# Performance work log

Measured on AMD Instinct MI355X. Metric: run time of the kernel, lower is better.

The kernel has to match this reference:

```python
import jax, jax.numpy as jnp
import numpy as np

B, T, F, H, E, L = 8192, 32, 64, 128, 16, 8


def _lstm_layer(x, wih, whh, bih, bhh):
    # x: [B, T, in]; weights in torch layout: wih [4H, in], whh [4H, H]
    b, t, _ = x.shape
    h_dim = whh.shape[1]
    pre = jnp.einsum('bti,gi->btg', x, wih) + bih + bhh  # [B, T, 4H]
    pre_t = jnp.swapaxes(pre, 0, 1)  # [T, B, 4H]

    def step(carry, p):
        h, c = carry
        g = p + h @ whh.T
        i, f, gg, o = jnp.split(g, 4, axis=-1)  # torch gate order: i, f, g, o
        i = jax.nn.sigmoid(i)
        f = jax.nn.sigmoid(f)
        gg = jnp.tanh(gg)
        o = jax.nn.sigmoid(o)
        c = f * c + i * gg
        h = o * jnp.tanh(c)
        return (h, c), h

    init = (jnp.zeros((b, h_dim), x.dtype), jnp.zeros((b, h_dim), x.dtype))
    _, ys = jax.lax.scan(step, init, pre_t)
    return jnp.swapaxes(ys, 0, 1)  # [B, T, H]


def setup_inputs() -> dict:
    key = jax.random.key(0)
    ks = jax.random.split(key, 32)

    def w(k, shape, fan_in):
        return (jax.random.uniform(k, shape, jnp.float32, -1.0, 1.0) / np.sqrt(fan_in)).astype(jnp.float32)

    inp = {
        'x_feat': jax.random.normal(ks[0], (B, T, 8), jnp.float32),
        'access_type': jax.random.randint(ks[1], (B, T), 0, 16),
        # MemoryPatternEncoder
        'de_w1': w(ks[2], (32, 8), 8), 'de_b1': w(ks[3], (32,), 8),
        'de_w2': w(ks[4], (F, 32), 32), 'de_b2': w(ks[5], (F,), 32),
        'embed': jax.random.normal(ks[6], (E, 16), jnp.float32),
        'comb_w': w(ks[7], (F, F + 16), F + 16), 'comb_b': w(ks[8], (F,), F + 16),
        # 2-layer LSTM (torch param layout)
        'lstm0_wih': w(ks[9], (4 * H, F), H), 'lstm0_whh': w(ks[10], (4 * H, H), H),
        'lstm0_bih': w(ks[11], (4 * H,), H), 'lstm0_bhh': w(ks[12], (4 * H,), H),
        'lstm1_wih': w(ks[13], (4 * H, H), H), 'lstm1_whh': w(ks[14], (4 * H, H), H),
        'lstm1_bih': w(ks[15], (4 * H,), H), 'lstm1_bhh': w(ks[16], (4 * H,), H),
        # delta_predictor: H -> H -> L
        'dp_w1': w(ks[17], (H, H), H), 'dp_b1': w(ks[18], (H,), H),
        'dp_w2': w(ks[19], (L, H), H), 'dp_b2': w(ks[20], (L,), H),
        # confidence_predictor: H -> H//2 -> L, sigmoid
        'cp_w1': w(ks[21], (H // 2, H), H), 'cp_b1': w(ks[22], (H // 2,), H),
        'cp_w2': w(ks[23], (L, H // 2), H // 2), 'cp_b2': w(ks[24], (L,), H // 2),
        # pattern_classifier: H -> 32 -> 4, softmax
        'pc_w1': w(ks[25], (32, H), H), 'pc_b1': w(ks[26], (32,), H),
        'pc_w2': w(ks[27], (4, 32), 32), 'pc_b2': w(ks[28], (4,), 32),
    }
    return inp


def reference(x_feat, access_type, de_w1, de_b1, de_w2, de_b2, embed, comb_w, comb_b,
              lstm0_wih, lstm0_whh, lstm0_bih, lstm0_bhh,
              lstm1_wih, lstm1_whh, lstm1_bih, lstm1_bhh,
              dp_w1, dp_b1, dp_w2, dp_b2, cp_w1, cp_b1, cp_w2, cp_b2,
              pc_w1, pc_b1, pc_w2, pc_b2):
    # --- MemoryPatternEncoder (batched over B, T) ---
    delta_feat = jax.nn.relu(x_feat @ de_w1.T + de_b1) @ de_w2.T + de_b2  # [B,T,F]
    access_feat = embed[access_type]  # [B,T,16]
    feats = jnp.concatenate([delta_feat, access_feat], axis=-1) @ comb_w.T + comb_b  # [B,T,F]

    # --- 2-layer LSTM (dropout inactive: inference/no_grad path) ---
    y0 = _lstm_layer(feats, lstm0_wih, lstm0_whh, lstm0_bih, lstm0_bhh)
    y1 = _lstm_layer(y0, lstm1_wih, lstm1_whh, lstm1_bih, lstm1_bhh)
    h = y1[:, -1, :]  # final hidden [B,H]

    # --- heads ---
    deltas = (jax.nn.relu(h @ dp_w1.T + dp_b1) @ dp_w2.T + dp_b2) * 1000000.0  # [B,L]
    conf = jax.nn.sigmoid(jax.nn.relu(h @ cp_w1.T + cp_b1) @ cp_w2.T + cp_b2)  # [B,L]
    probs = jax.nn.softmax(jax.nn.relu(h @ pc_w1.T + pc_b1) @ pc_w2.T + pc_b2, axis=-1)  # [B,4]
    return jnp.concatenate([deltas, conf, probs], axis=-1)  # [B, 2L+4]
```

## Files before the change

### kernel.cpp

```cpp
#include <hip/hip_runtime.h>
#include <hip/hip_bf16.h>

typedef short s8v __attribute__((ext_vector_type(8)));
typedef float f4v __attribute__((ext_vector_type(4)));

#define DEV __device__ __forceinline__

DEV unsigned short f2b(float f) {
  unsigned u = __builtin_bit_cast(unsigned, f);
  u += 0x7FFFu + ((u >> 16) & 1u);
  return (unsigned short)(u >> 16);
}
DEV float b2f(unsigned short s) {
  unsigned u = ((unsigned)s) << 16;
  return __builtin_bit_cast(float, u);
}
DEV float sigf(float x) { return __builtin_amdgcn_rcpf(1.f + __expf(-x)); }
DEV float tanhf_(float x) { return 1.f - 2.f * __builtin_amdgcn_rcpf(__expf(2.f * x) + 1.f); }

#define O_WHH0  0u
#define O_WHH1  131072u
#define O_WIH0  262144u
#define O_WIH1  327680u
#define O_B0    458752u
#define O_B1    460800u
#define O_WA    462848u
#define O_EMB2  471040u
#define O_BC    475136u
#define O_W1F   475392u
#define O_DP2T  532736u
#define O_FEATS 4733696u
#define O_Y0    38288128u

#define P_WHH   0
#define P_H0    131072
#define P_H1    139264
#define P_TOT   147456
#define P_HMID  0
#define P_HW2   29696
#define P_HPC   36864

DEV int orig_col(int c) { return 128 * ((c >> 4) & 3) + 16 * (c >> 6) + (c & 15); }

__global__ void prep_kernel(
    const float* de_w1, const float* de_b1, const float* de_w2, const float* de_b2,
    const float* embed, const float* comb_w, const float* comb_b,
    const float* w0ih, const float* w0hh, const float* b0ih, const float* b0hh,
    const float* w1ih, const float* w1hh, const float* b1ih, const float* b1hh,
    const float* dp_w1, const float* dp_w2, const float* cp_w1, const float* cp_w2,
    const float* pc_w1, const float* pc_w2, char* ws)
{
  unsigned short* wih0p = (unsigned short*)(ws + O_WIH0);
  unsigned short* whh0p = (unsigned short*)(ws + O_WHH0);
  unsigned short* wih1p = (unsigned short*)(ws + O_WIH1);
  unsigned short* whh1p = (unsigned short*)(ws + O_WHH1);
  float* b0p = (float*)(ws + O_B0);
  float* b1p = (float*)(ws + O_B1);
  float* Wa  = (float*)(ws + O_WA);
  float* bc  = (float*)(ws + O_BC);
  float* em2 = (float*)(ws + O_EMB2);
  unsigned short* w1f = (unsigned short*)(ws + O_W1F);
  float* dp2t = (float*)(ws + O_DP2T);
  float* cp2t = dp2t + 1024;
  float* pc2t = dp2t + 1536;

  const int T0 = 32768, T1 = T0 + 65536, T2 = T1 + 65536, T3 = T2 + 65536,
            T4 = T3 + 512, T5 = T4 + 512, T6 = T5 + 2048, T7 = T6 + 64,
            T8 = T7 + 1024, T9 = T8 + 28672, T10 = T9 + 1024, T11 = T10 + 512,
            T12 = T11 + 128;

  for (int idx = blockIdx.x * 256 + threadIdx.x; idx < T12; idx += gridDim.x * 256) {
    if (idx < T3) {
      int u, Kin; const float* src; unsigned short* dst;
      if (idx < T0)      { u = idx;      Kin = 64;  src = w0ih; dst = wih0p; }
      else if (idx < T1) { u = idx - T0; Kin = 128; src = w0hh; dst = whh0p; }
      else if (idx < T2) { u = idx - T1; Kin = 128; src = w1ih; dst = wih1p; }
      else               { u = idx - T2; Kin = 128; src = w1hh; dst = whh1p; }
      int j = u & 7, l = (u >> 3) & 63, nt = (u >> 9) & 31, kt = u >> 14;
      int c = 16 * nt + (l & 15);
      int k = 32 * kt + 8 * (l >> 4) + j;
      dst[u] = f2b(src[orig_col(c) * Kin + k]);
    } else if (idx < T5) {
      int u = idx - T3;
      if (u < 512) b0p[u] = b0ih[orig_col(u)] + b0hh[orig_col(u)];
      else { int c = u - 512; b1p[c] = b1ih[orig_col(c)] + b1hh[orig_col(c)]; }
    } else if (idx < T6) {
      int u = idx - T5, f = u >> 5, kk = u & 31;
      float a = 0.f;
      for (int f2 = 0; f2 < 64; f2++) a += comb_w[f * 80 + f2] * de_w2[f2 * 32 + kk];
      Wa[u] = a;
    } else if (idx < T7) {
      int f = idx - T6;
      float a = comb_b[f];
      for (int f2 = 0; f2 < 64; f2++) a += comb_w[f * 80 + f2] * de_b2[f2];
      bc[f] = a;
    } else if (idx < T8) {
      int u = idx - T7, e = u >> 6, f = u & 63;
      float a = 0.f;
      for (int j = 0; j < 16; j++) a += embed[e * 16 + j] * comb_w[f * 80 + 64 + j];
      em2[u] = a;
    } else if (idx < T9) {
      int u = idx - T8;
      int j = u & 7, l = (u >> 3) & 63, kt = (u >> 9) & 3, nt = u >> 11;
      int c = 16 * nt + (l & 15);
      int k = 32 * kt + 8 * (l >> 4) + j;
      float v;
      if (c < 128)      v = dp_w1[c * 128 + k];
      else if (c < 192) v = cp_w1[(c - 128) * 128 + k];
      else              v = pc_w1[(c - 192) * 128 + k];
      w1f[u] = f2b(v);
    }
    else if (idx < T10)   { int u = idx - T9;  int k = u >> 3, o = u & 7; dp2t[u] = dp_w2[o * 128 + k]; }
    else if (idx < T11)   { int u = idx - T10; int k = u >> 3, o = u & 7; cp2t[u] = cp_w2[o * 64 + k]; }
    else                  { int u = idx - T11; int k = u >> 2, o = u & 3; pc2t[u] = pc_w2[o * 32 + k]; }
  }
}

__global__ __launch_bounds__(256) void frontend_kernel(
    const float* __restrict__ x_feat, const int* __restrict__ acc_t,
    const float* __restrict__ de_w1, const float* __restrict__ de_b1,
    const char* __restrict__ ws, unsigned short* __restrict__ feats)
{
  __shared__ float sW1[256], sB1[32], sWa[2048], sBc[64], sE2T[1024];
  const float* Wa  = (const float*)(ws + O_WA);
  const float* bc  = (const float*)(ws + O_BC);
  const float* em2 = (const float*)(ws + O_EMB2);
  int tid = threadIdx.x;
  sW1[tid] = de_w1[tid];
  if (tid < 32) sB1[tid] = de_b1[tid];
  for (int i = tid; i < 2048; i += 256) sWa[i] = Wa[i];
  if (tid < 64) sBc[tid] = bc[tid];
  for (int i = tid; i < 1024; i += 256) sE2T[i] = em2[(i & 15) * 64 + (i >> 4)];
  __syncthreads();

  int g = blockIdx.x * 256 + tid;
  f4v x0 = ((const f4v*)(x_feat + (size_t)g * 8))[0];
  f4v x1 = ((const f4v*)(x_feat + (size_t)g * 8))[1];
  float xs[8];
#pragma unroll
  for (int i = 0; i < 4; i++) { xs[i] = x0[i]; xs[4 + i] = x1[i]; }
  int at = acc_t[g];

  float r1[32];
#pragma unroll
  for (int kk = 0; kk < 32; kk++) {
    float a = sB1[kk];
#pragma unroll
    for (int i = 0; i < 8; i++) a += xs[i] * sW1[kk * 8 + i];
    r1[kk] = fmaxf(a, 0.f);
  }
  unsigned short* dst = feats + (size_t)g * 64;
  for (int j8 = 0; j8 < 8; j8++) {
    s8v pack;
#pragma unroll
    for (int jj = 0; jj < 8; jj++) {
      int j = j8 * 8 + jj;
      float a = sBc[j] + sE2T[j * 16 + at];
      const f4v* wr = (const f4v*)(sWa + j * 32);
#pragma unroll
      for (int k4 = 0; k4 < 8; k4++) {
        f4v wv = wr[k4];
        a += r1[4 * k4 + 0] * wv[0] + r1[4 * k4 + 1] * wv[1] +
             r1[4 * k4 + 2] * wv[2] + r1[4 * k4 + 3] * wv[3];
      }
      pack[jj] = (short)f2b(a);
    }
    *(s8v*)(dst + j8 * 8) = pack;
  }
}

template <int PASS>
DEV void run_pass(int tid, int blk,
                  const unsigned short* __restrict__ whhp,
                  const unsigned short* __restrict__ wihp,
                  const float* __restrict__ bp,
                  const unsigned short* __restrict__ inglob,
                  unsigned short* __restrict__ y0buf,
                  unsigned short* sWhh, unsigned short* sH0, unsigned short* sH1)
{
  constexpr int KIN = PASS ? 128 : 64;
  constexpr int NKT = KIN / 32;
  const int w = tid >> 6, l = tid & 63, l15 = l & 15, lhi = l >> 4;
  const int d = 16 * w + l15;

  auto aoff = [&](int t, int mt, int kt) -> size_t {
    int row = 16 * mt + l15;
    if constexpr (PASS == 0)
      return ((size_t)(blk * 32 + row) * 32 + t) * 64 + 32 * kt + 8 * lhi;
    else
      return (size_t)blk * 131072 + (size_t)t * 4096 + row * 128 + 32 * kt + 8 * lhi;
  };

  s8v A0[2][NKT], A1[2][NKT];
#pragma unroll
  for (int mt = 0; mt < 2; mt++)
#pragma unroll
    for (int kt = 0; kt < NKT; kt++)
      A0[mt][kt] = *(const s8v*)(inglob + aoff(0, mt, kt));

  for (int i = tid; i < 8192; i += 512)
    *(s8v*)(sWhh + i * 8) = *(const s8v*)(whhp + i * 8);
  { s8v z = {0, 0, 0, 0, 0, 0, 0, 0}; *(s8v*)(sH0 + tid * 8) = z; }

  s8v wf[NKT][4];
#pragma unroll
  for (int kt = 0; kt < NKT; kt++)
#pragma unroll
    for (int gg = 0; gg < 4; gg++)
      wf[kt][gg] = *(const s8v*)(wihp + ((size_t)(kt * 32 + 4 * w + gg) * 64 + l) * 8);

  float bias_[4];
#pragma unroll
  for (int gg = 0; gg < 4; gg++) bias_[gg] = bp[64 * w + 16 * gg + l15];
  float cst[2][4] = {{0, 0, 0, 0}, {0, 0, 0, 0}};

  const int yrow = tid >> 4, yq = tid & 15;
  const size_t ybase = (size_t)blk * 131072 + yrow * 128 + ((yq ^ (yrow & 7)) * 8);
  const int yldsb = yrow * 256 + yq * 16;

  __syncthreads();

#define LSTM_STEP(T, AC, AN, HRD, HWR)                                          \
  {                                                                             \
    const int tn_ = (T) < 31 ? (T) + 1 : 31;                                    \
    _Pragma("unroll")                                                           \
    for (int mt = 0; mt < 2; mt++)                                              \
      _Pragma("unroll")                                                         \
      for (int kt = 0; kt < NKT; kt++)                                          \
        AN[mt][kt] = *(const s8v*)(inglob + aoff(tn_, mt, kt));                 \
    if (PASS == 0 && (T) > 0) {                                                 \
      s8v hv8 = *(const s8v*)((const char*)(HRD) + yldsb);                      \
      *(s8v*)(y0buf + ybase + (size_t)((T) - 1) * 4096) = hv8;                  \
    }                                                                           \
    f4v acc[2][4];                                                              \
    _Pragma("unroll")                                                           \
    for (int mt = 0; mt < 2; mt++)                                              \
      _Pragma("unroll")                                                         \
      for (int gg = 0; gg < 4; gg++)                                            \
        acc[mt][gg] = f4v{bias_[gg], bias_[gg], bias_[gg], bias_[gg]};          \
    _Pragma("unroll")                                                           \
    for (int kt = 0; kt < NKT; kt++)                                            \
      _Pragma("unroll")                                                         \
      for (int mt = 0; mt < 2; mt++)                                            \
        _Pragma("unroll")                                                       \
        for (int gg = 0; gg < 4; gg++)                                          \
          acc[mt][gg] = __builtin_amdgcn_mfma_f32_16x16x32_bf16(                \
              AC[mt][kt], wf[kt][gg], acc[mt][gg], 0, 0, 0);                    \
    _Pragma("unroll")                                                           \
    for (int kt = 0; kt < 4; kt++) {                                            \
      s8v bfr[4];                                                               \
      _Pragma("unroll")                                                         \
      for (int gg = 0; gg < 4; gg++)                                            \
        bfr[gg] = *(const s8v*)(sWhh + (size_t)((kt * 32 + 4 * w + gg) * 64 + l) * 8); \
      _Pragma("unroll")                                                         \
      for (int mt = 0; mt < 2; mt++) {                                          \
        int row = 16 * mt + l15;                                                \
        s8v ha = *(const s8v*)((const char*)(HRD) + row * 256 +                 \
                               ((kt * 64 + lhi * 16) ^ ((row & 7) << 4)));      \
        _Pragma("unroll")                                                       \
        for (int gg = 0; gg < 4; gg++)                                          \
          acc[mt][gg] = __builtin_amdgcn_mfma_f32_16x16x32_bf16(                \
              ha, bfr[gg], acc[mt][gg], 0, 0, 0);                               \
      }                                                                         \
    }                                                                           \
    _Pragma("unroll")                                                           \
    for (int mt = 0; mt < 2; mt++)                                              \
      _Pragma("unroll")                                                         \
      for (int r = 0; r < 4; r++) {                                             \
        float iv = sigf(acc[mt][0][r]);                                         \
        float fv = sigf(acc[mt][1][r]);                                         \
        float gv = tanhf_(acc[mt][2][r]);                                       \
        float ov = sigf(acc[mt][3][r]);                                         \
        float cv = fv * cst[mt][r] + iv * gv;                                   \
        cst[mt][r] = cv;                                                        \
        float hv = ov * tanhf_(cv);                                             \
        int row = 16 * mt + 4 * lhi + r;                                        \
        *(unsigned short*)((char*)(HWR) + row * 256 +                           \
                           ((d * 2) ^ ((row & 7) << 4))) = f2b(hv);             \
      }                                                                         \
    __syncthreads();                                                            \
  }

  for (int th = 0; th < 16; ++th) {
    LSTM_STEP(2 * th,     A0, A1, sH0, sH1)
    LSTM_STEP(2 * th + 1, A1, A0, sH1, sH0)
  }
#undef LSTM_STEP

  if (PASS == 0) {
    s8v hv8 = *(const s8v*)((const char*)sH0 + yldsb);
    *(s8v*)(y0buf + ybase + (size_t)31 * 4096) = hv8;
  }
}

DEV void heads_phase(int tid, int blk, char* pool, const char* ws,
                     const float* __restrict__ dp_b1, const float* __restrict__ dp_b2,
                     const float* __restrict__ cp_b1, const float* __restrict__ cp_b2,
                     const float* __restrict__ pc_b1, const float* __restrict__ pc_b2,
                     float* __restrict__ out)
{
  const int w = tid >> 6, l = tid & 63, l15 = l & 15, lhi = l >> 4;
  float* smid = (float*)(pool + P_HMID);
  float* sw2  = (float*)(pool + P_HW2);
  float* spc  = (float*)(pool + P_HPC);
  const char* sH0 = pool + P_H0;

  for (int i = tid; i < 1664; i += 512) sw2[i] = ((const float*)(ws + O_DP2T))[i];

  if (w < 7) {
    const unsigned short* w1f = (const unsigned short*)(ws + O_W1F);
    s8v bf[2][4];
#pragma unroll
    for (int nn = 0; nn < 2; nn++)
#pragma unroll
      for (int kt = 0; kt < 4; kt++)
        bf[nn][kt] = *(const s8v*)(w1f + (size_t)(((2 * w + nn) * 4 + kt) * 64 + l) * 8);

    const f4v z4 = {0.f, 0.f, 0.f, 0.f};
    f4v acc[2][2];
#pragma unroll
    for (int kt = 0; kt < 4; kt++)
#pragma unroll
      for (int mt = 0; mt < 2; mt++) {
        int row = 16 * mt + l15;
        s8v ha = *(const s8v*)(sH0 + row * 256 + ((kt * 64 + lhi * 16) ^ ((row & 7) << 4)));
#pragma unroll
        for (int nn = 0; nn < 2; nn++)
          acc[nn][mt] = __builtin_amdgcn_mfma_f32_16x16x32_bf16(
              ha, bf[nn][kt], kt == 0 ? z4 : acc[nn][mt], 0, 0, 0);
      }

#pragma unroll
    for (int nn = 0; nn < 2; nn++) {
      int c = 16 * (2 * w + nn) + l15;
      float b1v = (c < 128) ? dp_b1[c] : ((c < 192) ? cp_b1[c - 128] : pc_b1[c - 192]);
#pragma unroll
      for (int mt = 0; mt < 2; mt++)
#pragma unroll
        for (int r = 0; r < 4; r++) {
          int row = 16 * mt + 4 * lhi + r;
          smid[row * 228 + c] = fmaxf(acc[nn][mt][r] + b1v, 0.f);
        }
    }
  }
  __syncthreads();

  for (int i = tid; i < 640; i += 512) {
    int row = i / 20, o = i - row * 20;
    const float* mr = smid + row * 228;
    if (o < 8) {
      float a = dp_b2[o];
      for (int k = 0; k < 128; k++) a += mr[k] * sw2[k * 8 + o];
      out[(size_t)(blk * 32 + row) * 20 + o] = a * 1e6f;
    } else if (o < 16) {
      int oo = o - 8; float a = cp_b2[oo];
      for (int k = 0; k < 64; k++) a += mr[128 + k] * sw2[1024 + k * 8 + oo];
      out[(size_t)(blk * 32 + row) * 20 + o] = sigf(a);
    } else {
      int oo = o - 16; float a = pc_b2[oo];
      for (int k = 0; k < 32; k++) a += mr[192 + k] * sw2[1536 + k * 4 + oo];
      spc[row * 4 + oo] = a;
    }
  }
  __syncthreads();

  if (tid < 32) {
    int row = tid;
    float v0 = spc[row * 4], v1 = spc[row * 4 + 1], v2 = spc[row * 4 + 2], v3 = spc[row * 4 + 3];
    float m = fmaxf(fmaxf(v0, v1), fmaxf(v2, v3));
    float e0 = __expf(v0 - m), e1 = __expf(v1 - m), e2 = __expf(v2 - m), e3 = __expf(v3 - m);
    float rs = __builtin_amdgcn_rcpf(e0 + e1 + e2 + e3);
    size_t base = (size_t)(blk * 32 + row) * 20 + 16;
    out[base] = e0 * rs; out[base + 1] = e1 * rs; out[base + 2] = e2 * rs; out[base + 3] = e3 * rs;
  }
}

__global__ __launch_bounds__(512, 2) void lstm_main(
    const char* __restrict__ ws_c, char* __restrict__ ws,
    const float* __restrict__ dp_b1, const float* __restrict__ dp_b2,
    const float* __restrict__ cp_b1, const float* __restrict__ cp_b2,
    const float* __restrict__ pc_b1, const float* __restrict__ pc_b2,
    float* __restrict__ out)
{
  __shared__ __align__(16) char pool[P_TOT];
  int tid = threadIdx.x, blk = blockIdx.x;
  unsigned short* sWhh = (unsigned short*)(pool + P_WHH);
  unsigned short* sH0  = (unsigned short*)(pool + P_H0);
  unsigned short* sH1  = (unsigned short*)(pool + P_H1);

  run_pass<0>(tid, blk,
              (const unsigned short*)(ws_c + O_WHH0), (const unsigned short*)(ws_c + O_WIH0),
              (const float*)(ws_c + O_B0),
              (const unsigned short*)(ws_c + O_FEATS),
              (unsigned short*)(ws + O_Y0),
              sWhh, sH0, sH1);
  __syncthreads();
  run_pass<1>(tid, blk,
              (const unsigned short*)(ws_c + O_WHH1), (const unsigned short*)(ws_c + O_WIH1),
              (const float*)(ws_c + O_B1),
              (const unsigned short*)(ws + O_Y0),
              nullptr,
              sWhh, sH0, sH1);
  __syncthreads();
  heads_phase(tid, blk, pool, ws_c, dp_b1, dp_b2, cp_b1, cp_b2, pc_b1, pc_b2, out);
}

extern "C" void kernel_launch(void* const* d_in, const int* in_sizes, int n_in,
                              void* d_out, int out_size, void* d_ws, size_t ws_size,
                              hipStream_t stream) {
  const float* x_feat = (const float*)d_in[0];
  const int*   acc_t  = (const int*)d_in[1];
  const float* de_w1 = (const float*)d_in[2],  *de_b1 = (const float*)d_in[3];
  const float* de_w2 = (const float*)d_in[4],  *de_b2 = (const float*)d_in[5];
  const float* embed = (const float*)d_in[6];
  const float* comb_w = (const float*)d_in[7], *comb_b = (const float*)d_in[8];
  const float* w0ih = (const float*)d_in[9],  *w0hh = (const float*)d_in[10];
  const float* b0ih = (const float*)d_in[11], *b0hh = (const float*)d_in[12];
  const float* w1ih = (const float*)d_in[13], *w1hh = (const float*)d_in[14];
  const float* b1ih = (const float*)d_in[15], *b1hh = (const float*)d_in[16];
  const float* dp_w1 = (const float*)d_in[17], *dp_b1 = (const float*)d_in[18];
  const float* dp_w2 = (const float*)d_in[19], *dp_b2 = (const float*)d_in[20];
  const float* cp_w1 = (const float*)d_in[21], *cp_b1 = (const float*)d_in[22];
  const float* cp_w2 = (const float*)d_in[23], *cp_b2 = (const float*)d_in[24];
  const float* pc_w1 = (const float*)d_in[25], *pc_b1 = (const float*)d_in[26];
  const float* pc_w2 = (const float*)d_in[27], *pc_b2 = (const float*)d_in[28];
  char* ws = (char*)d_ws;

  prep_kernel<<<256, 256, 0, stream>>>(
      de_w1, de_b1, de_w2, de_b2, embed, comb_w, comb_b,
      w0ih, w0hh, b0ih, b0hh, w1ih, w1hh, b1ih, b1hh,
      dp_w1, dp_w2, cp_w1, cp_w2, pc_w1, pc_w2, ws);

  frontend_kernel<<<1024, 256, 0, stream>>>(
      x_feat, acc_t, de_w1, de_b1, ws, (unsigned short*)(ws + O_FEATS));

  lstm_main<<<256, 512, 0, stream>>>(
      ws, ws, dp_b1, dp_b2, cp_b1, cp_b2, pc_b1, pc_b2, (float*)d_out);
}
```

Measured before the change: 204.7 us.

## Keep recurrent weights in registers and fold bias into exp2 gate math

```diff
diff --git a/kernel.cpp b/kernel.cpp
--- a/kernel.cpp
+++ b/kernel.cpp
@@ -5,6 +5,7 @@
 typedef float f4v __attribute__((ext_vector_type(4)));
 
 #define DEV __device__ __forceinline__
+#define LOG2E 1.4426950408889634f
 
 DEV unsigned short f2b(float f) {
   unsigned u = __builtin_bit_cast(unsigned, f);
@@ -16,7 +17,6 @@
   return __builtin_bit_cast(float, u);
 }
 DEV float sigf(float x) { return __builtin_amdgcn_rcpf(1.f + __expf(-x)); }
-DEV float tanhf_(float x) { return 1.f - 2.f * __builtin_amdgcn_rcpf(__expf(2.f * x) + 1.f); }
 
 #define O_WHH0  0u
 #define O_WHH1  131072u
@@ -32,13 +32,12 @@
 #define O_FEATS 4733696u
 #define O_Y0    38288128u
 
-#define P_WHH   0
-#define P_H0    131072
-#define P_H1    139264
-#define P_TOT   147456
-#define P_HMID  0
-#define P_HW2   29696
-#define P_HPC   36864
+#define P_H0    0
+#define P_H1    8192
+#define P_HMID  16384
+#define P_HW2   45568
+#define P_HPC   52224
+#define P_TOT   52736
 
 DEV int orig_col(int c) { return 128 * ((c >> 4) & 3) + 16 * (c >> 6) + (c & 15); }
 
@@ -176,12 +175,12 @@
                   const float* __restrict__ bp,
                   const unsigned short* __restrict__ inglob,
                   unsigned short* __restrict__ y0buf,
-                  unsigned short* sWhh, unsigned short* sH0, unsigned short* sH1)
+                  char* pool)
 {
-  constexpr int KIN = PASS ? 128 : 64;
-  constexpr int NKT = KIN / 32;
+  constexpr int NKT = PASS ? 4 : 2;
   const int w = tid >> 6, l = tid & 63, l15 = l & 15, lhi = l >> 4;
   const int d = 16 * w + l15;
+  unsigned short* sH0 = (unsigned short*)(pool + P_H0);
 
   auto aoff = [&](int t, int mt, int kt) -> size_t {
     int row = 16 * mt + l15;
@@ -198,21 +197,26 @@
     for (int kt = 0; kt < NKT; kt++)
       A0[mt][kt] = *(const s8v*)(inglob + aoff(0, mt, kt));
 
-  for (int i = tid; i < 8192; i += 512)
-    *(s8v*)(sWhh + i * 8) = *(const s8v*)(whhp + i * 8);
   { s8v z = {0, 0, 0, 0, 0, 0, 0, 0}; *(s8v*)(sH0 + tid * 8) = z; }
 
-  s8v wf[NKT][4];
+  s8v wf[NKT][4], bfr[4][4];
 #pragma unroll
   for (int kt = 0; kt < NKT; kt++)
 #pragma unroll
     for (int gg = 0; gg < 4; gg++)
       wf[kt][gg] = *(const s8v*)(wihp + ((size_t)(kt * 32 + 4 * w + gg) * 64 + l) * 8);
-
-  float bias_[4];
-#pragma unroll
-  for (int gg = 0; gg < 4; gg++) bias_[gg] = bp[64 * w + 16 * gg + l15];
+#pragma unroll
+  for (int kt = 0; kt < 4; kt++)
+#pragma unroll
+    for (int gg = 0; gg < 4; gg++)
+      bfr[kt][gg] = *(const s8v*)(whhp + ((size_t)(kt * 32 + 4 * w + gg) * 64 + l) * 8);
+
+  const float nbi2 = -bp[64 * w + l15] * LOG2E,
+              nbf2 = -bp[64 * w + 16 + l15] * LOG2E,
+              bg2  = 2.f * LOG2E * bp[64 * w + 32 + l15],
+              nbo2 = -bp[64 * w + 48 + l15] * LOG2E;
   float cst[2][4] = {{0, 0, 0, 0}, {0, 0, 0, 0}};
+  const f4v z4 = {0.f, 0.f, 0.f, 0.f};
 
   const int yrow = tid >> 4, yq = tid & 15;
   const size_t ybase = (size_t)blk * 131072 + yrow * 128 + ((yq ^ (yrow & 7)) * 8);
@@ -237,9 +241,10 @@
     for (int mt = 0; mt < 2; mt++)                                              \
       _Pragma("unroll")                                                         \
       for (int gg = 0; gg < 4; gg++)                                            \
-        acc[mt][gg] = f4v{bias_[gg], bias_[gg], bias_[gg], bias_[gg]};          \
+        acc[mt][gg] = __builtin_amdgcn_mfma_f32_16x16x32_bf16(                  \
+            AC[mt][0], wf[0][gg], z4, 0, 0, 0);                                 \
     _Pragma("unroll")                                                           \
-    for (int kt = 0; kt < NKT; kt++)                                            \
+    for (int kt = 1; kt < NKT; kt++)                                            \
       _Pragma("unroll")                                                         \
       for (int mt = 0; mt < 2; mt++)                                            \
         _Pragma("unroll")                                                       \
@@ -247,11 +252,7 @@
           acc[mt][gg] = __builtin_amdgcn_mfma_f32_16x16x32_bf16(                \
               AC[mt][kt], wf[kt][gg], acc[mt][gg], 0, 0, 0);                    \
     _Pragma("unroll")                                                           \
-    for (int kt = 0; kt < 4; kt++) {                                            \
-      s8v bfr[4];                                                               \
-      _Pragma("unroll")                                                         \
-      for (int gg = 0; gg < 4; gg++)                                            \
-        bfr[gg] = *(const s8v*)(sWhh + (size_t)((kt * 32 + 4 * w + gg) * 64 + l) * 8); \
+    for (int kt = 0; kt < 4; kt++)                                              \
       _Pragma("unroll")                                                         \
       for (int mt = 0; mt < 2; mt++) {                                          \
         int row = 16 * mt + l15;                                                \
@@ -260,20 +261,24 @@
         _Pragma("unroll")                                                       \
         for (int gg = 0; gg < 4; gg++)                                          \
           acc[mt][gg] = __builtin_amdgcn_mfma_f32_16x16x32_bf16(                \
-              ha, bfr[gg], acc[mt][gg], 0, 0, 0);                               \
+              ha, bfr[kt][gg], acc[mt][gg], 0, 0, 0);                           \
       }                                                                         \
-    }                                                                           \
     _Pragma("unroll")                                                           \
     for (int mt = 0; mt < 2; mt++)                                              \
       _Pragma("unroll")                                                         \
       for (int r = 0; r < 4; r++) {                                             \
-        float iv = sigf(acc[mt][0][r]);                                         \
-        float fv = sigf(acc[mt][1][r]);                                         \
-        float gv = tanhf_(acc[mt][2][r]);                                       \
-        float ov = sigf(acc[mt][3][r]);                                         \
-        float cv = fv * cst[mt][r] + iv * gv;                                   \
+        float xi = acc[mt][0][r], xf = acc[mt][1][r],                           \
+              xg = acc[mt][2][r], xo = acc[mt][3][r];                           \
+        float iv = __builtin_amdgcn_rcpf(1.f + exp2f(fmaf(xi, -LOG2E, nbi2)));  \
+        float fv = __builtin_amdgcn_rcpf(1.f + exp2f(fmaf(xf, -LOG2E, nbf2)));  \
+        float ov = __builtin_amdgcn_rcpf(1.f + exp2f(fmaf(xo, -LOG2E, nbo2)));  \
+        float eg = exp2f(fmaf(xg, 2.f * LOG2E, bg2));                           \
+        float gv = fmaf(-2.f, __builtin_amdgcn_rcpf(eg + 1.f), 1.f);            \
+        float cv = fmaf(fv, cst[mt][r], iv * gv);                               \
         cst[mt][r] = cv;                                                        \
-        float hv = ov * tanhf_(cv);                                             \
+        float ec = exp2f(cv * (2.f * LOG2E));                                   \
+        float th = fmaf(-2.f, __builtin_amdgcn_rcpf(ec + 1.f), 1.f);            \
+        float hv = ov * th;                                                     \
         int row = 16 * mt + 4 * lhi + r;                                        \
         *(unsigned short*)((char*)(HWR) + row * 256 +                           \
                            ((d * 2) ^ ((row & 7) << 4))) = f2b(hv);             \
@@ -281,6 +286,7 @@
     __syncthreads();                                                            \
   }
 
+  unsigned short* sH1 = (unsigned short*)(pool + P_H1);
   for (int th = 0; th < 16; ++th) {
     LSTM_STEP(2 * th,     A0, A1, sH0, sH1)
     LSTM_STEP(2 * th + 1, A1, A0, sH1, sH0)
@@ -375,7 +381,8 @@
   }
 }
 
-__global__ __launch_bounds__(512, 2) void lstm_main(
+__global__ __launch_bounds__(512) __attribute__((amdgpu_waves_per_eu(1, 2)))
+void lstm_main(
     const char* __restrict__ ws_c, char* __restrict__ ws,
     const float* __restrict__ dp_b1, const float* __restrict__ dp_b2,
     const float* __restrict__ cp_b1, const float* __restrict__ cp_b2,
@@ -384,23 +391,18 @@
 {
   __shared__ __align__(16) char pool[P_TOT];
   int tid = threadIdx.x, blk = blockIdx.x;
-  unsigned short* sWhh = (unsigned short*)(pool + P_WHH);
-  unsigned short* sH0  = (unsigned short*)(pool + P_H0);
-  unsigned short* sH1  = (unsigned short*)(pool + P_H1);
 
   run_pass<0>(tid, blk,
               (const unsigned short*)(ws_c + O_WHH0), (const unsigned short*)(ws_c + O_WIH0),
               (const float*)(ws_c + O_B0),
               (const unsigned short*)(ws_c + O_FEATS),
-              (unsigned short*)(ws + O_Y0),
-              sWhh, sH0, sH1);
+              (unsigned short*)(ws + O_Y0), pool);
   __syncthreads();
   run_pass<1>(tid, blk,
               (const unsigned short*)(ws_c + O_WHH1), (const unsigned short*)(ws_c + O_WIH1),
               (const float*)(ws_c + O_B1),
               (const unsigned short*)(ws + O_Y0),
-              nullptr,
-              sWhh, sH0, sH1);
+              nullptr, pool);
   __syncthreads();
   heads_phase(tid, blk, pool, ws_c, dp_b1, dp_b2, cp_b1, cp_b2, pc_b1, pc_b2, out);
 }
```

Result: slower. 212.1 us (+3.6%).

## Hold recurrent Whh fragments in AGPRs instead of staging through LDS

Applied to the files above, without the earlier changes.

```diff
diff --git a/kernel.cpp b/kernel.cpp
--- a/kernel.cpp
+++ b/kernel.cpp
@@ -32,13 +32,12 @@
 #define O_FEATS 4733696u
 #define O_Y0    38288128u
 
-#define P_WHH   0
-#define P_H0    131072
-#define P_H1    139264
-#define P_TOT   147456
-#define P_HMID  0
-#define P_HW2   29696
-#define P_HPC   36864
+#define P_H0    0
+#define P_H1    8192
+#define P_HMID  16384
+#define P_HW2   45568
+#define P_HPC   52224
+#define P_TOT   52736
 
 DEV int orig_col(int c) { return 128 * ((c >> 4) & 3) + 16 * (c >> 6) + (c & 15); }
 
@@ -176,7 +175,7 @@
                   const float* __restrict__ bp,
                   const unsigned short* __restrict__ inglob,
                   unsigned short* __restrict__ y0buf,
-                  unsigned short* sWhh, unsigned short* sH0, unsigned short* sH1)
+                  unsigned short* sH0, unsigned short* sH1)
 {
   constexpr int KIN = PASS ? 128 : 64;
   constexpr int NKT = KIN / 32;
@@ -198,8 +197,6 @@
     for (int kt = 0; kt < NKT; kt++)
       A0[mt][kt] = *(const s8v*)(inglob + aoff(0, mt, kt));
 
-  for (int i = tid; i < 8192; i += 512)
-    *(s8v*)(sWhh + i * 8) = *(const s8v*)(whhp + i * 8);
   { s8v z = {0, 0, 0, 0, 0, 0, 0, 0}; *(s8v*)(sH0 + tid * 8) = z; }
 
   s8v wf[NKT][4];
@@ -208,6 +205,13 @@
 #pragma unroll
     for (int gg = 0; gg < 4; gg++)
       wf[kt][gg] = *(const s8v*)(wihp + ((size_t)(kt * 32 + 4 * w + gg) * 64 + l) * 8);
+
+  s8v whhA[4][4];
+#pragma unroll
+  for (int kt = 0; kt < 4; kt++)
+#pragma unroll
+    for (int gg = 0; gg < 4; gg++)
+      whhA[kt][gg] = *(const s8v*)(whhp + ((size_t)(kt * 32 + 4 * w + gg) * 64 + l) * 8);
 
   float bias_[4];
 #pragma unroll
@@ -247,11 +251,7 @@
           acc[mt][gg] = __builtin_amdgcn_mfma_f32_16x16x32_bf16(                \
               AC[mt][kt], wf[kt][gg], acc[mt][gg], 0, 0, 0);                    \
     _Pragma("unroll")                                                           \
-    for (int kt = 0; kt < 4; kt++) {                                            \
-      s8v bfr[4];                                                               \
-      _Pragma("unroll")                                                         \
-      for (int gg = 0; gg < 4; gg++)                                            \
-        bfr[gg] = *(const s8v*)(sWhh + (size_t)((kt * 32 + 4 * w + gg) * 64 + l) * 8); \
+    for (int kt = 0; kt < 4; kt++)                                              \
       _Pragma("unroll")                                                         \
       for (int mt = 0; mt < 2; mt++) {                                          \
         int row = 16 * mt + l15;                                                \
@@ -259,10 +259,15 @@
                                ((kt * 64 + lhi * 16) ^ ((row & 7) << 4)));      \
         _Pragma("unroll")                                                       \
         for (int gg = 0; gg < 4; gg++)                                          \
-          acc[mt][gg] = __builtin_amdgcn_mfma_f32_16x16x32_bf16(                \
-              ha, bfr[gg], acc[mt][gg], 0, 0, 0);                               \
+          asm("v_mfma_f32_16x16x32_bf16 %0, %1, %2, %0"                         \
+              : "+v"(acc[mt][gg])                                               \
+              : "v"(ha), "a"(whhA[kt][gg]));                                    \
       }                                                                         \
-    }                                                                           \
+     \
+     \
+    asm volatile("s_nop 0xf\n\ts_nop 0xf"                                       \
+        : "+v"(acc[0][0]), "+v"(acc[0][1]), "+v"(acc[0][2]), "+v"(acc[0][3]),   \
+          "+v"(acc[1][0]), "+v"(acc[1][1]), "+v"(acc[1][2]), "+v"(acc[1][3]));  \
     _Pragma("unroll")                                                           \
     for (int mt = 0; mt < 2; mt++)                                              \
       _Pragma("unroll")                                                         \
@@ -384,23 +389,22 @@
 {
   __shared__ __align__(16) char pool[P_TOT];
   int tid = threadIdx.x, blk = blockIdx.x;
-  unsigned short* sWhh = (unsigned short*)(pool + P_WHH);
-  unsigned short* sH0  = (unsigned short*)(pool + P_H0);
-  unsigned short* sH1  = (unsigned short*)(pool + P_H1);
+  unsigned short* sH0 = (unsigned short*)(pool + P_H0);
+  unsigned short* sH1 = (unsigned short*)(pool + P_H1);
 
   run_pass<0>(tid, blk,
               (const unsigned short*)(ws_c + O_WHH0), (const unsigned short*)(ws_c + O_WIH0),
               (const float*)(ws_c + O_B0),
               (const unsigned short*)(ws_c + O_FEATS),
               (unsigned short*)(ws + O_Y0),
-              sWhh, sH0, sH1);
+              sH0, sH1);
   __syncthreads();
   run_pass<1>(tid, blk,
               (const unsigned short*)(ws_c + O_WHH1), (const unsigned short*)(ws_c + O_WIH1),
               (const float*)(ws_c + O_B1),
               (const unsigned short*)(ws + O_Y0),
               nullptr,
-              sWhh, sH0, sH1);
+              sH0, sH1);
   __syncthreads();
   heads_phase(tid, blk, pool, ws_c, dp_b1, dp_b2, cp_b1, cp_b2, pc_b1, pc_b2, out);
 }
```

Result: slower. 285.6 us (+39.5%).
